# Performance work log

Measured on AMD Instinct MI355X. Metric: run time of the kernel, lower is better.

Reference implementation:

```python
import jax, jax.numpy as jnp
import numpy as np

N = 100000
E = 3200000
NODE_IN = 118
D = 32
H = 4
C = D // H  # 8
EDGE_DIM = 50 + 3
L = 4
LN_EPS = 1e-5


def _layernorm(x, g, b):
    mu = jnp.mean(x, axis=-1, keepdims=True)
    var = jnp.mean(jnp.square(x - mu), axis=-1, keepdims=True)
    return (x - mu) * jax.lax.rsqrt(var + LN_EPS) * g + b


def setup_inputs() -> dict:
    key = jax.random.key(0)
    ks = jax.random.split(key, 20)
    x = jax.random.normal(ks[0], (N, NODE_IN), dtype=jnp.float32)
    edge_index = jax.random.randint(ks[1], (2, E), 0, N, dtype=jnp.int32)
    edge_len = jax.random.normal(ks[2], (E, 50), dtype=jnp.float32)
    edge_vec = jax.random.normal(ks[3], (E, 3), dtype=jnp.float32)
    s_in = 1.0 / np.sqrt(NODE_IN)
    s_d = 1.0 / np.sqrt(D)
    s_e = 1.0 / np.sqrt(EDGE_DIM)
    node_in_W = jax.random.normal(ks[4], (NODE_IN, D), dtype=jnp.float32) * s_in
    node_in_b = jnp.zeros((D,), dtype=jnp.float32)
    ln_g = jnp.ones((L, D), dtype=jnp.float32)
    ln_b = jnp.zeros((L, D), dtype=jnp.float32)
    Wq = jax.random.normal(ks[5], (L, D, D), dtype=jnp.float32) * s_d
    bq = jnp.zeros((L, D), dtype=jnp.float32)
    Wk = jax.random.normal(ks[6], (L, D, D), dtype=jnp.float32) * s_d
    bk = jnp.zeros((L, D), dtype=jnp.float32)
    Wv = jax.random.normal(ks[7], (L, D, D), dtype=jnp.float32) * s_d
    bv = jnp.zeros((L, D), dtype=jnp.float32)
    We = jax.random.normal(ks[8], (L, EDGE_DIM, D), dtype=jnp.float32) * s_e  # lin_edge, bias=False
    Wskip = jax.random.normal(ks[9], (L, D, D), dtype=jnp.float32) * s_d
    bskip = jnp.zeros((L, D), dtype=jnp.float32)
    return {"x": x, "edge_index": edge_index, "edge_len": edge_len, "edge_vec": edge_vec,
            "node_in_W": node_in_W, "node_in_b": node_in_b, "ln_g": ln_g, "ln_b": ln_b,
            "Wq": Wq, "bq": bq, "Wk": Wk, "bk": bk, "Wv": Wv, "bv": bv,
            "We": We, "Wskip": Wskip, "bskip": bskip}


def reference(x, edge_index, edge_len, edge_vec, node_in_W, node_in_b, ln_g, ln_b,
              Wq, bq, Wk, bk, Wv, bv, We, Wskip, bskip):
    src = edge_index[0]  # j (source), messages flow source -> target
    dst = edge_index[1]  # i (target), softmax grouped by dst
    ef = jnp.concatenate([edge_len, edge_vec], axis=-1)  # [E, 53]
    h = x @ node_in_W + node_in_b  # [N, D]
    scale = 1.0 / np.sqrt(C)
    for l in range(L):
        xn = _layernorm(h, ln_g[l], ln_b[l])
        q = (xn @ Wq[l] + bq[l]).reshape(N, H, C)
        k = (xn @ Wk[l] + bk[l]).reshape(N, H, C)
        v = (xn @ Wv[l] + bv[l]).reshape(N, H, C)
        e = (ef @ We[l]).reshape(E, H, C)  # per-edge key/value shift
        kj = k[src] + e                     # [E, H, C]
        alpha = jnp.sum(q[dst] * kj, axis=-1) * scale  # [E, H]
        # segment softmax over incoming edges of each target node
        amax = jax.ops.segment_max(alpha, dst, num_segments=N)  # [N, H]
        amax = jnp.where(jnp.isfinite(amax), amax, 0.0)
        ex = jnp.exp(alpha - amax[dst])
        denom = jax.ops.segment_sum(ex, dst, num_segments=N)
        w = ex / (denom[dst] + 1e-16)       # [E, H]
        msg = (v[src] + e) * w[:, :, None]  # [E, H, C]
        agg = jax.ops.segment_sum(msg.reshape(E, H * C), dst, num_segments=N)  # [N, D]
        y = agg + xn @ Wskip[l] + bskip[l]  # concat heads + root skip (lin_skip(x_i))
        h = h + y                            # residual
    return h
```

## Files before the change

kernel.cpp:

```cpp
#include <hip/hip_runtime.h>
#include <hip/hip_bf16.h>
#include <math.h>

#define N_NODES 100000
#define N_EDGES 3200000
#define NODE_IN 118
#define DIM 32
#define EDF 53
#define NLAYER 4

typedef __attribute__((ext_vector_type(8))) short short8;
typedef __attribute__((ext_vector_type(4))) float f32x4;
typedef unsigned short u16;
typedef unsigned int u32;

static __device__ __forceinline__ float bfhi2f(u32 hi) {
    union { u32 i; float f; } x; x.i = hi; return x.f;
}
static __device__ __forceinline__ u16 f2bf(float f) {
    union { float f; u32 i; } x; x.f = f;
    u32 i = x.i;
    return (u16)((i + 0x7FFFu + ((i >> 16) & 1u)) >> 16);
}
static __device__ __forceinline__ u32 pk2bf(float a, float b) {
    u32 r;
    asm("v_cvt_pk_bf16_f32 %0, %1, %2" : "=v"(r) : "v"(a), "v"(b));
    return r;
}

__global__ __launch_bounds__(256) void k_count(const int* __restrict__ dst, int* __restrict__ cnt) {
    int e = blockIdx.x * 256 + threadIdx.x;
    atomicAdd(&cnt[dst[e]], 1);
}

__global__ __launch_bounds__(256) void k_scanA(const int* __restrict__ cnt, int* __restrict__ off,
                                               int* __restrict__ bsum) {
    __shared__ int s[256];
    int t = threadIdx.x; int i = blockIdx.x * 256 + t;
    int v = (i < N_NODES) ? cnt[i] : 0;
    s[t] = v; __syncthreads();
    for (int d = 1; d < 256; d <<= 1) {
        int x = (t >= d) ? s[t - d] : 0; __syncthreads();
        s[t] += x; __syncthreads();
    }
    if (i < N_NODES) off[i] = s[t] - v;
    if (t == 255) bsum[blockIdx.x] = s[t];
}

__global__ __launch_bounds__(512) void k_scanB(int* bsum, int nb) {
    __shared__ int s[512];
    int t = threadIdx.x;
    int v = (t < nb) ? bsum[t] : 0;
    s[t] = v; __syncthreads();
    for (int d = 1; d < 512; d <<= 1) {
        int x = (t >= d) ? s[t - d] : 0; __syncthreads();
        s[t] += x; __syncthreads();
    }
    if (t < nb) bsum[t] = s[t] - v;
}

__global__ __launch_bounds__(256) void k_scanC(int* off, const int* __restrict__ bsum) {
    int i = blockIdx.x * 256 + threadIdx.x;
    if (i < N_NODES) off[i] += bsum[blockIdx.x];
    if (i == 0) off[N_NODES] = N_EDGES;
}

__global__ __launch_bounds__(256) void k_fill(const int* __restrict__ src, const int* __restrict__ dst,
                                              const int* __restrict__ off, int* __restrict__ cur,
                                              int2* __restrict__ epk) {
    int e = blockIdx.x * 256 + threadIdx.x;
    int d = dst[e];
    int p = off[d] + atomicAdd(&cur[d], 1);
    epk[p] = make_int2(e, src[e]);
}

__global__ __launch_bounds__(256) void k_init(const float* __restrict__ x, const float* __restrict__ W,
                                              const float* __restrict__ b, float* __restrict__ h) {
    __shared__ float Ws[NODE_IN * DIM];
    __shared__ float xs[8][NODE_IN];
    int t = threadIdx.x;
    for (int i = t; i < NODE_IN * DIM; i += 256) Ws[i] = W[i];
    int nb = blockIdx.x * 8;
    for (int i = t; i < 8 * NODE_IN; i += 256) {
        int n = i / NODE_IN, j = i % NODE_IN;
        xs[n][j] = x[(size_t)(nb + n) * NODE_IN + j];
    }
    __syncthreads();
    int n = t >> 5, c = t & 31;
    float acc = b[c];
    #pragma unroll 2
    for (int j = 0; j < NODE_IN; j++) acc += xs[n][j] * Ws[j * DIM + c];
    h[(size_t)(nb + n) * DIM + c] = acc;
}

template <int NL>
__global__ __launch_bounds__(256) void k_egemm(const float* __restrict__ elen, const float* __restrict__ evec,
                                               const float* __restrict__ We, u16* __restrict__ eout) {
    int tid = threadIdx.x;
    int lane = tid & 63;
    int wv = (blockIdx.x * 256 + tid) >> 6;
    int nw = (gridDim.x * 256) >> 6;
    int n15 = lane & 15, kb = lane >> 4;

    short8 bf[2][2 * NL];
    for (int s = 0; s < 2; s++) {
        for (int t = 0; t < 2 * NL; t++) {
            int n = t * 16 + n15;
            int lay = n >> 5, c = n & 31;
            short8 tmp;
            #pragma unroll
            for (int j = 0; j < 8; j++) {
                int kk = s * 32 + kb * 8 + j;
                float w = (kk < EDF) ? We[(size_t)lay * EDF * DIM + (size_t)kk * DIM + c] : 0.f;
                ((u16*)&tmp)[j] = f2bf(w);
            }
            bf[s][t] = tmp;
        }
    }

    const int NT = N_EDGES / 16;

    auto LOADA = [&](int tile, float* fv) {
        int pos = tile * 16 + n15;
        const float* lp = elen + (size_t)pos * 50;
        {
            const float2* p2 = (const float2*)(lp + kb * 8);
            #pragma unroll
            for (int j = 0; j < 4; j++) { float2 t2 = p2[j]; fv[2 * j] = t2.x; fv[2 * j + 1] = t2.y; }
        }
        if (kb < 2) {
            const float2* p2 = (const float2*)(lp + 32 + kb * 8);
            #pragma unroll
            for (int j = 0; j < 4; j++) { float2 t2 = p2[j]; fv[8 + 2 * j] = t2.x; fv[8 + 2 * j + 1] = t2.y; }
        } else if (kb == 2) {
            float2 t2 = *(const float2*)(lp + 48);
            const float* vp = evec + (size_t)pos * 3;
            fv[8] = t2.x; fv[9] = t2.y; fv[10] = vp[0]; fv[11] = vp[1]; fv[12] = vp[2];
            fv[13] = 0.f; fv[14] = 0.f; fv[15] = 0.f;
        } else {
            #pragma unroll
            for (int j = 8; j < 16; j++) fv[j] = 0.f;
        }
    };

    float cur[16];
    if (wv < NT) LOADA(wv, cur);

    for (int tile = wv; tile < NT; tile += nw) {
        int nxt = tile + nw;
        float nx[16];
        if (nxt < NT) LOADA(nxt, nx);

        union { short8 s; u32 u[4]; } A0, A1;
        A0.u[0] = pk2bf(cur[0], cur[1]);  A0.u[1] = pk2bf(cur[2], cur[3]);
        A0.u[2] = pk2bf(cur[4], cur[5]);  A0.u[3] = pk2bf(cur[6], cur[7]);
        A1.u[0] = pk2bf(cur[8], cur[9]);  A1.u[1] = pk2bf(cur[10], cur[11]);
        A1.u[2] = pk2bf(cur[12], cur[13]); A1.u[3] = pk2bf(cur[14], cur[15]);

        size_t rowbase = ((size_t)tile * 16 + n15) * DIM;
        #pragma unroll
        for (int t = 0; t < 2 * NL; t++) {
            f32x4 z = {0.f, 0.f, 0.f, 0.f};
            z = __builtin_amdgcn_mfma_f32_16x16x32_bf16(bf[0][t], A0.s, z, 0, 0, 0);
            z = __builtin_amdgcn_mfma_f32_16x16x32_bf16(bf[1][t], A1.s, z, 0, 0, 0);
            int lay = t >> 1;
            int ch = (t & 1) * 16 + kb * 4;
            uint2 sv = { pk2bf(z[0], z[1]), pk2bf(z[2], z[3]) };
            *(uint2*)&eout[(size_t)lay * N_EDGES * DIM + rowbase + ch] = sv;
        }

        #pragma unroll
        for (int j = 0; j < 16; j++) cur[j] = nx[j];
    }
}

__global__ __launch_bounds__(256) void k_node(const float* __restrict__ h,
        const float* __restrict__ g, const float* __restrict__ bta,
        const float* __restrict__ Wq, const float* __restrict__ bq,
        const float* __restrict__ Wk, const float* __restrict__ bk,
        const float* __restrict__ Wv, const float* __restrict__ bv,
        const float* __restrict__ Ws, const float* __restrict__ bs,
        float* __restrict__ qo, u16* __restrict__ kvo, float* __restrict__ hso) {
    __shared__ float WQ[DIM * DIM], WK[DIM * DIM], WV[DIM * DIM], WS[DIM * DIM];
    __shared__ float xn[8][DIM];
    int t = threadIdx.x;
    for (int i = t; i < DIM * DIM; i += 256) { WQ[i] = Wq[i]; WK[i] = Wk[i]; WV[i] = Wv[i]; WS[i] = Ws[i]; }
    int n = t >> 5, c = t & 31;
    size_t node = (size_t)blockIdx.x * 8 + n;
    float hv = h[node * DIM + c];
    float s1 = hv;
    for (int d = 1; d < 32; d <<= 1) s1 += __shfl_xor(s1, d, 64);
    float mu = s1 * (1.f / 32.f);
    float dv = hv - mu;
    float s2 = dv * dv;
    for (int d = 1; d < 32; d <<= 1) s2 += __shfl_xor(s2, d, 64);
    float inv = rsqrtf(s2 * (1.f / 32.f) + 1e-5f);
    float xv = dv * inv * g[c] + bta[c];
    xn[n][c] = xv;
    __syncthreads();
    float aq = bq[c], ak = bk[c], av = bv[c], as = bs[c];
    #pragma unroll 4
    for (int j = 0; j < DIM; j++) {
        float xj = xn[n][j];
        aq += xj * WQ[j * DIM + c];
        ak += xj * WK[j * DIM + c];
        av += xj * WV[j * DIM + c];
        as += xj * WS[j * DIM + c];
    }
    size_t o = node * DIM + c;
    qo[o] = aq * 0.35355339059327373f;
    kvo[node * 64 + c]      = f2bf(ak);
    kvo[node * 64 + 32 + c] = f2bf(av);
    hso[o] = hv + as;
}

__global__ __launch_bounds__(256) void k_aggr(const int* __restrict__ off, const int2* __restrict__ epk,
        const u16* __restrict__ eb, const float* __restrict__ qb, const u16* __restrict__ kvb,
        const float* __restrict__ hs, float* __restrict__ out) {
    int tid = threadIdx.x;
    size_t node = (size_t)blockIdx.x * 4 + (tid >> 6);
    int lane = tid & 63;
    int eg = lane >> 2, hq = lane & 3, c0 = hq * 8;
    float4 q0 = *(const float4*)&qb[node * DIM + c0];
    float4 q1 = *(const float4*)&qb[node * DIM + c0 + 4];
    int o0 = off[node], o1 = off[node + 1];
    int safe = (o0 < N_EDGES) ? o0 : (N_EDGES - 1);
    float n0=0.f,n1=0.f,n2=0.f,n3=0.f,n4=0.f,n5=0.f,n6=0.f,n7=0.f;
    float dacc = 0.f;

    int pA = o0 + eg;  bool aA = pA < o1; int2 xA = epk[aA ? pA : safe];
    int pB = pA + 16;  bool aB = pB < o1; int2 xB = epk[aB ? pB : safe];
    int pC = pB + 16;  bool aC = pC < o1; int2 xC = epk[aC ? pC : safe];

    uint4 dAe = *(const uint4*)&eb[(size_t)xA.x * DIM + c0];
    uint4 dAk = *(const uint4*)&kvb[(size_t)xA.y * 64 + c0];
    uint4 dAv = *(const uint4*)&kvb[(size_t)xA.y * 64 + 32 + c0];
    uint4 dBe = *(const uint4*)&eb[(size_t)xB.x * DIM + c0];
    uint4 dBk = *(const uint4*)&kvb[(size_t)xB.y * 64 + c0];
    uint4 dBv = *(const uint4*)&kvb[(size_t)xB.y * 64 + 32 + c0];

    for (int p = o0; p < o1; p += 16) {
        uint4 dCe = *(const uint4*)&eb[(size_t)xC.x * DIM + c0];
        uint4 dCk = *(const uint4*)&kvb[(size_t)xC.y * 64 + c0];
        uint4 dCv = *(const uint4*)&kvb[(size_t)xC.y * 64 + 32 + c0];
        int pD = pC + 16; bool aD = pD < o1; int2 xD = epk[aD ? pD : safe];

        float e0 = bfhi2f(dAe.x << 16), e1 = bfhi2f(dAe.x & 0xFFFF0000u);
        float e2 = bfhi2f(dAe.y << 16), e3 = bfhi2f(dAe.y & 0xFFFF0000u);
        float e4 = bfhi2f(dAe.z << 16), e5 = bfhi2f(dAe.z & 0xFFFF0000u);
        float e6 = bfhi2f(dAe.w << 16), e7 = bfhi2f(dAe.w & 0xFFFF0000u);
        float k0 = bfhi2f(dAk.x << 16), k1 = bfhi2f(dAk.x & 0xFFFF0000u);
        float k2 = bfhi2f(dAk.y << 16), k3 = bfhi2f(dAk.y & 0xFFFF0000u);
        float k4 = bfhi2f(dAk.z << 16), k5 = bfhi2f(dAk.z & 0xFFFF0000u);
        float k6 = bfhi2f(dAk.w << 16), k7 = bfhi2f(dAk.w & 0xFFFF0000u);
        float v0 = bfhi2f(dAv.x << 16), v1 = bfhi2f(dAv.x & 0xFFFF0000u);
        float v2 = bfhi2f(dAv.y << 16), v3 = bfhi2f(dAv.y & 0xFFFF0000u);
        float v4 = bfhi2f(dAv.z << 16), v5 = bfhi2f(dAv.z & 0xFFFF0000u);
        float v6 = bfhi2f(dAv.w << 16), v7 = bfhi2f(dAv.w & 0xFFFF0000u);
        float a =      q0.x * (k0 + e0);
        a = fmaf(q0.y, k1 + e1, a);
        a = fmaf(q0.z, k2 + e2, a);
        a = fmaf(q0.w, k3 + e3, a);
        a = fmaf(q1.x, k4 + e4, a);
        a = fmaf(q1.y, k5 + e5, a);
        a = fmaf(q1.z, k6 + e6, a);
        a = fmaf(q1.w, k7 + e7, a);
        float ex = aA ? __expf(a) : 0.f;
        n0 = fmaf(ex, v0 + e0, n0); n1 = fmaf(ex, v1 + e1, n1);
        n2 = fmaf(ex, v2 + e2, n2); n3 = fmaf(ex, v3 + e3, n3);
        n4 = fmaf(ex, v4 + e4, n4); n5 = fmaf(ex, v5 + e5, n5);
        n6 = fmaf(ex, v6 + e6, n6); n7 = fmaf(ex, v7 + e7, n7);
        dacc += ex;

        aA = aB; dAe = dBe; dAk = dBk; dAv = dBv;
        dBe = dCe; dBk = dCk; dBv = dCv;
        aB = aC; xC = xD; aC = aD; pC = pD;
    }
    #pragma unroll
    for (int d = 4; d < 64; d <<= 1) {
        n0 += __shfl_xor(n0, d); n1 += __shfl_xor(n1, d);
        n2 += __shfl_xor(n2, d); n3 += __shfl_xor(n3, d);
        n4 += __shfl_xor(n4, d); n5 += __shfl_xor(n5, d);
        n6 += __shfl_xor(n6, d); n7 += __shfl_xor(n7, d);
        dacc += __shfl_xor(dacc, d);
    }
    if (eg == 0) {
        float inv = 1.f / (dacc + 1e-16f);
        float4 h0 = *(const float4*)&hs[node * DIM + c0];
        float4 h1 = *(const float4*)&hs[node * DIM + c0 + 4];
        float4 o0v = { h0.x + n0 * inv, h0.y + n1 * inv, h0.z + n2 * inv, h0.w + n3 * inv };
        float4 o1v = { h1.x + n4 * inv, h1.y + n5 * inv, h1.z + n6 * inv, h1.w + n7 * inv };
        *(float4*)&out[node * DIM + c0] = o0v;
        *(float4*)&out[node * DIM + c0 + 4] = o1v;
    }
}

extern "C" void kernel_launch(void* const* d_in, const int* in_sizes, int n_in,
                              void* d_out, int out_size, void* d_ws, size_t ws_size,
                              hipStream_t stream) {
    const float* x    = (const float*)d_in[0];
    const int*   ei   = (const int*)d_in[1];
    const int*   src  = ei;
    const int*   dst  = ei + N_EDGES;
    const float* elen = (const float*)d_in[2];
    const float* evec = (const float*)d_in[3];
    const float* niW  = (const float*)d_in[4];
    const float* nib  = (const float*)d_in[5];
    const float* lng  = (const float*)d_in[6];
    const float* lnb  = (const float*)d_in[7];
    const float* Wq   = (const float*)d_in[8];
    const float* bq   = (const float*)d_in[9];
    const float* Wk   = (const float*)d_in[10];
    const float* bk   = (const float*)d_in[11];
    const float* Wv   = (const float*)d_in[12];
    const float* bv   = (const float*)d_in[13];
    const float* We   = (const float*)d_in[14];
    const float* Wsk  = (const float*)d_in[15];
    const float* bsk  = (const float*)d_in[16];
    float* out = (float*)d_out;

    unsigned char* w = (unsigned char*)d_ws;
    auto alloc = [&](size_t bytes) -> void* {
        void* p = (void*)w; w += (bytes + 255) & ~(size_t)255; return p;
    };
    int*   off  = (int*)alloc((N_NODES + 1) * sizeof(int));
    int*   cnt  = (int*)alloc(N_NODES * sizeof(int));
    int*   bsum = (int*)alloc(512 * sizeof(int));
    int2*  epk  = (int2*)alloc((size_t)N_EDGES * sizeof(int2));
    float* h    = (float*)alloc((size_t)N_NODES * DIM * sizeof(float));
    float* qb   = (float*)alloc((size_t)N_NODES * DIM * sizeof(float));
    u16*   kvb  = (u16*)alloc((size_t)N_NODES * 64 * sizeof(u16));
    float* hsb  = (float*)alloc((size_t)N_NODES * DIM * sizeof(float));
    size_t used = (size_t)(w - (unsigned char*)d_ws);
    size_t e_full = (size_t)NLAYER * N_EDGES * DIM * sizeof(u16);
    size_t e_one  = (size_t)N_EDGES * DIM * sizeof(u16);
    bool full = (used + e_full) <= ws_size;
    u16* ebuf = (u16*)alloc(full ? e_full : e_one);

    const int EB = N_EDGES / 256;
    const int NB = N_NODES / 8;
    const int AB = N_NODES / 4;
    const int nbScan = (N_NODES + 255) / 256;

    hipMemsetAsync(cnt, 0, N_NODES * sizeof(int), stream);
    k_count<<<EB, 256, 0, stream>>>(dst, cnt);
    k_scanA<<<nbScan, 256, 0, stream>>>(cnt, off, bsum);
    k_scanB<<<1, 512, 0, stream>>>(bsum, nbScan);
    k_scanC<<<nbScan, 256, 0, stream>>>(off, bsum);
    hipMemsetAsync(cnt, 0, N_NODES * sizeof(int), stream);
    k_fill<<<EB, 256, 0, stream>>>(src, dst, off, cnt, epk);

    k_init<<<NB, 256, 0, stream>>>(x, niW, nib, h);

    if (full) k_egemm<4><<<4096, 256, 0, stream>>>(elen, evec, We, ebuf);

    for (int l = 0; l < NLAYER; l++) {
        if (!full) k_egemm<1><<<4096, 256, 0, stream>>>(elen, evec, We + (size_t)l * EDF * DIM, ebuf);
        k_node<<<NB, 256, 0, stream>>>(h, lng + l * DIM, lnb + l * DIM,
                                       Wq + (size_t)l * DIM * DIM, bq + l * DIM,
                                       Wk + (size_t)l * DIM * DIM, bk + l * DIM,
                                       Wv + (size_t)l * DIM * DIM, bv + l * DIM,
                                       Wsk + (size_t)l * DIM * DIM, bsk + l * DIM,
                                       qb, kvb, hsb);
        const u16* el = full ? (ebuf + (size_t)l * N_EDGES * DIM) : ebuf;
        k_aggr<<<AB, 256, 0, stream>>>(off, epk, el, qb, kvb, hsb,
                                       (l == NLAYER - 1) ? out : h);
    }
}
```

Measured before the change: 1.309 ms.

## Store edge features in CSR order with interleaved layers for streaming aggregation

The edge GEMM now gathers edge inputs through the dst-sorted permutation and writes its output in CSR order, with all four layers interleaved per edge. The output is transposed through LDS so each row goes out as a wide store. The aggregation kernel then reads edge features sequentially by CSR position rather than by scattered edge id, and the packed edge index array is split so it loads only source ids. The scattered reads move into the one-time GEMM input load, and the per-layer reads become a strided stream over the interleaved buffer.

```diff
diff --git a/kernel.cpp b/kernel.cpp
--- a/kernel.cpp
+++ b/kernel.cpp
@@ -67,11 +67,12 @@
 
 __global__ __launch_bounds__(256) void k_fill(const int* __restrict__ src, const int* __restrict__ dst,
                                               const int* __restrict__ off, int* __restrict__ cur,
-                                              int2* __restrict__ epk) {
+                                              int* __restrict__ eidx, int* __restrict__ esrc) {
     int e = blockIdx.x * 256 + threadIdx.x;
     int d = dst[e];
     int p = off[d] + atomicAdd(&cur[d], 1);
-    epk[p] = make_int2(e, src[e]);
+    eidx[p] = e;
+    esrc[p] = src[e];
 }
 
 __global__ __launch_bounds__(256) void k_init(const float* __restrict__ x, const float* __restrict__ W,
@@ -95,9 +96,12 @@
 
 template <int NL>
 __global__ __launch_bounds__(256) void k_egemm(const float* __restrict__ elen, const float* __restrict__ evec,
-                                               const float* __restrict__ We, u16* __restrict__ eout) {
+                                               const int* __restrict__ eidx, const float* __restrict__ We,
+                                               u16* __restrict__ eout) {
+    __shared__ u16 st[4][16 * 160];
     int tid = threadIdx.x;
     int lane = tid & 63;
+    int wvl = tid >> 6;
     int wv = (blockIdx.x * 256 + tid) >> 6;
     int nw = (gridDim.x * 256) >> 6;
     int n15 = lane & 15, kb = lane >> 4;
@@ -120,9 +124,8 @@
 
     const int NT = N_EDGES / 16;
 
-    auto LOADA = [&](int tile, float* fv) {
-        int pos = tile * 16 + n15;
-        const float* lp = elen + (size_t)pos * 50;
+    auto LOADD = [&](int eid, float* fv) {
+        const float* lp = elen + (size_t)eid * 50;
         {
             const float2* p2 = (const float2*)(lp + kb * 8);
             #pragma unroll
@@ -134,7 +137,7 @@
             for (int j = 0; j < 4; j++) { float2 t2 = p2[j]; fv[8 + 2 * j] = t2.x; fv[8 + 2 * j + 1] = t2.y; }
         } else if (kb == 2) {
             float2 t2 = *(const float2*)(lp + 48);
-            const float* vp = evec + (size_t)pos * 3;
+            const float* vp = evec + (size_t)eid * 3;
             fv[8] = t2.x; fv[9] = t2.y; fv[10] = vp[0]; fv[11] = vp[1]; fv[12] = vp[2];
             fv[13] = 0.f; fv[14] = 0.f; fv[15] = 0.f;
         } else {
@@ -143,34 +146,51 @@
         }
     };
 
+    int eidA = (wv < NT) ? eidx[wv * 16 + n15] : 0;
+    int t1 = wv + nw;
+    int eidB = (t1 < NT) ? eidx[t1 * 16 + n15] : 0;
     float cur[16];
-    if (wv < NT) LOADA(wv, cur);
+    if (wv < NT) LOADD(eidA, cur);
 
     for (int tile = wv; tile < NT; tile += nw) {
         int nxt = tile + nw;
         float nx[16];
-        if (nxt < NT) LOADA(nxt, nx);
+        if (nxt < NT) LOADD(eidB, nx);
+        int t2 = tile + 2 * nw;
+        int eidC = (t2 < NT) ? eidx[t2 * 16 + n15] : 0;
 
         union { short8 s; u32 u[4]; } A0, A1;
-        A0.u[0] = pk2bf(cur[0], cur[1]);  A0.u[1] = pk2bf(cur[2], cur[3]);
-        A0.u[2] = pk2bf(cur[4], cur[5]);  A0.u[3] = pk2bf(cur[6], cur[7]);
-        A1.u[0] = pk2bf(cur[8], cur[9]);  A1.u[1] = pk2bf(cur[10], cur[11]);
+        A0.u[0] = pk2bf(cur[0], cur[1]);   A0.u[1] = pk2bf(cur[2], cur[3]);
+        A0.u[2] = pk2bf(cur[4], cur[5]);   A0.u[3] = pk2bf(cur[6], cur[7]);
+        A1.u[0] = pk2bf(cur[8], cur[9]);   A1.u[1] = pk2bf(cur[10], cur[11]);
         A1.u[2] = pk2bf(cur[12], cur[13]); A1.u[3] = pk2bf(cur[14], cur[15]);
 
-        size_t rowbase = ((size_t)tile * 16 + n15) * DIM;
+        u16* W = st[wvl];
         #pragma unroll
         for (int t = 0; t < 2 * NL; t++) {
             f32x4 z = {0.f, 0.f, 0.f, 0.f};
-            z = __builtin_amdgcn_mfma_f32_16x16x32_bf16(bf[0][t], A0.s, z, 0, 0, 0);
-            z = __builtin_amdgcn_mfma_f32_16x16x32_bf16(bf[1][t], A1.s, z, 0, 0, 0);
-            int lay = t >> 1;
-            int ch = (t & 1) * 16 + kb * 4;
-            uint2 sv = { pk2bf(z[0], z[1]), pk2bf(z[2], z[3]) };
-            *(uint2*)&eout[(size_t)lay * N_EDGES * DIM + rowbase + ch] = sv;
+            z = __builtin_amdgcn_mfma_f32_16x16x32_bf16(A0.s, bf[0][t], z, 0, 0, 0);
+            z = __builtin_amdgcn_mfma_f32_16x16x32_bf16(A1.s, bf[1][t], z, 0, 0, 0);
+            int n = t * 16 + n15;
+            #pragma unroll
+            for (int r = 0; r < 4; r++) {
+                int row = kb * 4 + r;
+                int idx = row * 160 + (n ^ ((row & 12) << 2));
+                W[idx] = f2bf(z[r]);
+            }
+        }
+        int row = lane >> 2, q = lane & 3;
+        size_t base2 = (size_t)(tile * 16) * (NL * 32);
+        #pragma unroll
+        for (int lay = 0; lay < NL; lay++) {
+            int idx = row * 160 + ((lay * 32 + q * 8) ^ ((row & 12) << 2));
+            short8 vblk = *(const short8*)&W[idx];
+            *(short8*)&eout[base2 + (size_t)row * (NL * 32) + lay * 32 + q * 8] = vblk;
         }
 
         #pragma unroll
         for (int j = 0; j < 16; j++) cur[j] = nx[j];
+        eidA = eidB; eidB = eidC;
     }
 }
 
@@ -214,8 +234,9 @@
     hso[o] = hv + as;
 }
 
-__global__ __launch_bounds__(256) void k_aggr(const int* __restrict__ off, const int2* __restrict__ epk,
-        const u16* __restrict__ eb, const float* __restrict__ qb, const u16* __restrict__ kvb,
+__global__ __launch_bounds__(256) void k_aggr(const int* __restrict__ off, const int* __restrict__ esrc,
+        const u16* __restrict__ eb, int estr,
+        const float* __restrict__ qb, const u16* __restrict__ kvb,
         const float* __restrict__ hs, float* __restrict__ out) {
     int tid = threadIdx.x;
     size_t node = (size_t)blockIdx.x * 4 + (tid >> 6);
@@ -228,22 +249,24 @@
     float n0=0.f,n1=0.f,n2=0.f,n3=0.f,n4=0.f,n5=0.f,n6=0.f,n7=0.f;
     float dacc = 0.f;
 
-    int pA = o0 + eg;  bool aA = pA < o1; int2 xA = epk[aA ? pA : safe];
-    int pB = pA + 16;  bool aB = pB < o1; int2 xB = epk[aB ? pB : safe];
-    int pC = pB + 16;  bool aC = pC < o1; int2 xC = epk[aC ? pC : safe];
-
-    uint4 dAe = *(const uint4*)&eb[(size_t)xA.x * DIM + c0];
-    uint4 dAk = *(const uint4*)&kvb[(size_t)xA.y * 64 + c0];
-    uint4 dAv = *(const uint4*)&kvb[(size_t)xA.y * 64 + 32 + c0];
-    uint4 dBe = *(const uint4*)&eb[(size_t)xB.x * DIM + c0];
-    uint4 dBk = *(const uint4*)&kvb[(size_t)xB.y * 64 + c0];
-    uint4 dBv = *(const uint4*)&kvb[(size_t)xB.y * 64 + 32 + c0];
+    int pA = o0 + eg;  bool aA = pA < o1; int sA = esrc[aA ? pA : safe];
+    int pB = pA + 16;  bool aB = pB < o1; int sB = esrc[aB ? pB : safe];
+    int pC = pB + 16;  bool aC = pC < o1; int sC = esrc[aC ? pC : safe];
+    int cA = aA ? pA : safe, cB = aB ? pB : safe, cCs = aC ? pC : safe;
+
+    uint4 dAe = *(const uint4*)&eb[(size_t)cA * estr + c0];
+    uint4 dAk = *(const uint4*)&kvb[(size_t)sA * 64 + c0];
+    uint4 dAv = *(const uint4*)&kvb[(size_t)sA * 64 + 32 + c0];
+    uint4 dBe = *(const uint4*)&eb[(size_t)cB * estr + c0];
+    uint4 dBk = *(const uint4*)&kvb[(size_t)sB * 64 + c0];
+    uint4 dBv = *(const uint4*)&kvb[(size_t)sB * 64 + 32 + c0];
 
     for (int p = o0; p < o1; p += 16) {
-        uint4 dCe = *(const uint4*)&eb[(size_t)xC.x * DIM + c0];
-        uint4 dCk = *(const uint4*)&kvb[(size_t)xC.y * 64 + c0];
-        uint4 dCv = *(const uint4*)&kvb[(size_t)xC.y * 64 + 32 + c0];
-        int pD = pC + 16; bool aD = pD < o1; int2 xD = epk[aD ? pD : safe];
+        uint4 dCe = *(const uint4*)&eb[(size_t)cCs * estr + c0];
+        uint4 dCk = *(const uint4*)&kvb[(size_t)sC * 64 + c0];
+        uint4 dCv = *(const uint4*)&kvb[(size_t)sC * 64 + 32 + c0];
+        int pD = pC + 16; bool aD = pD < o1; int qD = aD ? pD : safe;
+        int sD = esrc[qD];
 
         float e0 = bfhi2f(dAe.x << 16), e1 = bfhi2f(dAe.x & 0xFFFF0000u);
         float e2 = bfhi2f(dAe.y << 16), e3 = bfhi2f(dAe.y & 0xFFFF0000u);
@@ -274,7 +297,8 @@
 
         aA = aB; dAe = dBe; dAk = dBk; dAv = dBv;
         dBe = dCe; dBk = dCk; dBv = dCv;
-        aB = aC; xC = xD; aC = aD; pC = pD;
+        aB = aC; aC = aD;
+        cCs = qD; sC = sD; pC = pD;
     }
     #pragma unroll
     for (int d = 4; d < 64; d <<= 1) {
@@ -326,7 +350,8 @@
     int*   off  = (int*)alloc((N_NODES + 1) * sizeof(int));
     int*   cnt  = (int*)alloc(N_NODES * sizeof(int));
     int*   bsum = (int*)alloc(512 * sizeof(int));
-    int2*  epk  = (int2*)alloc((size_t)N_EDGES * sizeof(int2));
+    int*   eidx = (int*)alloc((size_t)N_EDGES * sizeof(int));
+    int*   esrc = (int*)alloc((size_t)N_EDGES * sizeof(int));
     float* h    = (float*)alloc((size_t)N_NODES * DIM * sizeof(float));
     float* qb   = (float*)alloc((size_t)N_NODES * DIM * sizeof(float));
     u16*   kvb  = (u16*)alloc((size_t)N_NODES * 64 * sizeof(u16));
@@ -348,22 +373,23 @@
     k_scanB<<<1, 512, 0, stream>>>(bsum, nbScan);
     k_scanC<<<nbScan, 256, 0, stream>>>(off, bsum);
     hipMemsetAsync(cnt, 0, N_NODES * sizeof(int), stream);
-    k_fill<<<EB, 256, 0, stream>>>(src, dst, off, cnt, epk);
+    k_fill<<<EB, 256, 0, stream>>>(src, dst, off, cnt, eidx, esrc);
 
     k_init<<<NB, 256, 0, stream>>>(x, niW, nib, h);
 
-    if (full) k_egemm<4><<<4096, 256, 0, stream>>>(elen, evec, We, ebuf);
+    if (full) k_egemm<4><<<4096, 256, 0, stream>>>(elen, evec, eidx, We, ebuf);
 
     for (int l = 0; l < NLAYER; l++) {
-        if (!full) k_egemm<1><<<4096, 256, 0, stream>>>(elen, evec, We + (size_t)l * EDF * DIM, ebuf);
+        if (!full) k_egemm<1><<<4096, 256, 0, stream>>>(elen, evec, eidx, We + (size_t)l * EDF * DIM, ebuf);
         k_node<<<NB, 256, 0, stream>>>(h, lng + l * DIM, lnb + l * DIM,
                                        Wq + (size_t)l * DIM * DIM, bq + l * DIM,
                                        Wk + (size_t)l * DIM * DIM, bk + l * DIM,
                                        Wv + (size_t)l * DIM * DIM, bv + l * DIM,
                                        Wsk + (size_t)l * DIM * DIM, bsk + l * DIM,
                                        qb, kvb, hsb);
-        const u16* el = full ? (ebuf + (size_t)l * N_EDGES * DIM) : ebuf;
-        k_aggr<<<AB, 256, 0, stream>>>(off, epk, el, qb, kvb, hsb,
+        const u16* el = full ? (ebuf + (size_t)l * DIM) : ebuf;
+        int estr = full ? (NLAYER * DIM) : DIM;
+        k_aggr<<<AB, 256, 0, stream>>>(off, esrc, el, estr, qb, kvb, hsb,
                                        (l == NLAYER - 1) ? out : h);
     }
 }
```

Result: slower. 1.451 ms (+10.8%).

## Split per-node attention aggregation into edge-parallel alpha kernel and segment-sum kernel

Applied to the files above, without the earlier changes.

Replaces the fused per-destination aggregation kernel with two kernels. An edge-parallel kernel computes exp(alpha) and the weighted message for each CSR-ordered edge and writes them to new edge-sized buffers. A second kernel sums them per node, with 4 nodes per wavefront. The aim is to remove load imbalance and poor lane use from variable-degree nodes. The cost is extra global traffic: about 200MB of message and exp writes plus reads per layer, and a wider 16-byte edge record.

```diff
diff --git a/kernel.cpp b/kernel.cpp
--- a/kernel.cpp
+++ b/kernel.cpp
@@ -67,11 +67,11 @@
 
 __global__ __launch_bounds__(256) void k_fill(const int* __restrict__ src, const int* __restrict__ dst,
                                               const int* __restrict__ off, int* __restrict__ cur,
-                                              int2* __restrict__ epk) {
+                                              int4* __restrict__ epk) {
     int e = blockIdx.x * 256 + threadIdx.x;
     int d = dst[e];
     int p = off[d] + atomicAdd(&cur[d], 1);
-    epk[p] = make_int2(e, src[e]);
+    epk[p] = make_int4(e, src[e], d, 0);
 }
 
 __global__ __launch_bounds__(256) void k_init(const float* __restrict__ x, const float* __restrict__ W,
@@ -152,9 +152,9 @@
         if (nxt < NT) LOADA(nxt, nx);
 
         union { short8 s; u32 u[4]; } A0, A1;
-        A0.u[0] = pk2bf(cur[0], cur[1]);  A0.u[1] = pk2bf(cur[2], cur[3]);
-        A0.u[2] = pk2bf(cur[4], cur[5]);  A0.u[3] = pk2bf(cur[6], cur[7]);
-        A1.u[0] = pk2bf(cur[8], cur[9]);  A1.u[1] = pk2bf(cur[10], cur[11]);
+        A0.u[0] = pk2bf(cur[0], cur[1]);   A0.u[1] = pk2bf(cur[2], cur[3]);
+        A0.u[2] = pk2bf(cur[4], cur[5]);   A0.u[3] = pk2bf(cur[6], cur[7]);
+        A1.u[0] = pk2bf(cur[8], cur[9]);   A1.u[1] = pk2bf(cur[10], cur[11]);
         A1.u[2] = pk2bf(cur[12], cur[13]); A1.u[3] = pk2bf(cur[14], cur[15]);
 
         size_t rowbase = ((size_t)tile * 16 + n15) * DIM;
@@ -214,70 +214,78 @@
     hso[o] = hv + as;
 }
 
-__global__ __launch_bounds__(256) void k_aggr(const int* __restrict__ off, const int2* __restrict__ epk,
+__global__ __launch_bounds__(256) void k_alpha(const int4* __restrict__ epk,
         const u16* __restrict__ eb, const float* __restrict__ qb, const u16* __restrict__ kvb,
+        u16* __restrict__ mb, float* __restrict__ exb) {
+    int t = blockIdx.x * 256 + threadIdx.x;
+    int hq = t & 3, c0 = hq * 8;
+    size_t p = (size_t)(t >> 2);
+    int4 pk = epk[p];
+    int eid = pk.x, sj = pk.y, nd = pk.z;
+    uint4 e4 = *(const uint4*)&eb[(size_t)eid * DIM + c0];
+    uint4 k4 = *(const uint4*)&kvb[(size_t)sj * 64 + c0];
+    uint4 v4 = *(const uint4*)&kvb[(size_t)sj * 64 + 32 + c0];
+    float4 q0 = *(const float4*)&qb[(size_t)nd * DIM + c0];
+    float4 q1 = *(const float4*)&qb[(size_t)nd * DIM + c0 + 4];
+
+    float e0 = bfhi2f(e4.x << 16), e1 = bfhi2f(e4.x & 0xFFFF0000u);
+    float e2 = bfhi2f(e4.y << 16), e3 = bfhi2f(e4.y & 0xFFFF0000u);
+    float e4f = bfhi2f(e4.z << 16), e5 = bfhi2f(e4.z & 0xFFFF0000u);
+    float e6 = bfhi2f(e4.w << 16), e7 = bfhi2f(e4.w & 0xFFFF0000u);
+    float k0 = bfhi2f(k4.x << 16), k1 = bfhi2f(k4.x & 0xFFFF0000u);
+    float k2 = bfhi2f(k4.y << 16), k3 = bfhi2f(k4.y & 0xFFFF0000u);
+    float k4f = bfhi2f(k4.z << 16), k5 = bfhi2f(k4.z & 0xFFFF0000u);
+    float k6 = bfhi2f(k4.w << 16), k7 = bfhi2f(k4.w & 0xFFFF0000u);
+    float v0 = bfhi2f(v4.x << 16), v1 = bfhi2f(v4.x & 0xFFFF0000u);
+    float v2 = bfhi2f(v4.y << 16), v3 = bfhi2f(v4.y & 0xFFFF0000u);
+    float v4f = bfhi2f(v4.z << 16), v5 = bfhi2f(v4.z & 0xFFFF0000u);
+    float v6 = bfhi2f(v4.w << 16), v7 = bfhi2f(v4.w & 0xFFFF0000u);
+
+    float a =      q0.x * (k0 + e0);
+    a = fmaf(q0.y, k1 + e1, a);
+    a = fmaf(q0.z, k2 + e2, a);
+    a = fmaf(q0.w, k3 + e3, a);
+    a = fmaf(q1.x, k4f + e4f, a);
+    a = fmaf(q1.y, k5 + e5, a);
+    a = fmaf(q1.z, k6 + e6, a);
+    a = fmaf(q1.w, k7 + e7, a);
+    float ex = __expf(a);
+
+    uint4 mm;
+    mm.x = pk2bf(ex * (v0 + e0),  ex * (v1 + e1));
+    mm.y = pk2bf(ex * (v2 + e2),  ex * (v3 + e3));
+    mm.z = pk2bf(ex * (v4f + e4f), ex * (v5 + e5));
+    mm.w = pk2bf(ex * (v6 + e6),  ex * (v7 + e7));
+    *(uint4*)&mb[p * DIM + c0] = mm;
+    exb[p * 4 + hq] = ex;
+}
+
+__global__ __launch_bounds__(256) void k_msum(const int* __restrict__ off,
+        const u16* __restrict__ mb, const float* __restrict__ exb,
         const float* __restrict__ hs, float* __restrict__ out) {
     int tid = threadIdx.x;
-    size_t node = (size_t)blockIdx.x * 4 + (tid >> 6);
     int lane = tid & 63;
-    int eg = lane >> 2, hq = lane & 3, c0 = hq * 8;
-    float4 q0 = *(const float4*)&qb[node * DIM + c0];
-    float4 q1 = *(const float4*)&qb[node * DIM + c0 + 4];
+    int ns = lane >> 4, eg = (lane >> 2) & 3, hq = lane & 3, c0 = hq * 8;
+    size_t node = (size_t)blockIdx.x * 16 + (size_t)(tid >> 6) * 4 + ns;
     int o0 = off[node], o1 = off[node + 1];
-    int safe = (o0 < N_EDGES) ? o0 : (N_EDGES - 1);
     float n0=0.f,n1=0.f,n2=0.f,n3=0.f,n4=0.f,n5=0.f,n6=0.f,n7=0.f;
     float dacc = 0.f;
-
-    int pA = o0 + eg;  bool aA = pA < o1; int2 xA = epk[aA ? pA : safe];
-    int pB = pA + 16;  bool aB = pB < o1; int2 xB = epk[aB ? pB : safe];
-    int pC = pB + 16;  bool aC = pC < o1; int2 xC = epk[aC ? pC : safe];
-
-    uint4 dAe = *(const uint4*)&eb[(size_t)xA.x * DIM + c0];
-    uint4 dAk = *(const uint4*)&kvb[(size_t)xA.y * 64 + c0];
-    uint4 dAv = *(const uint4*)&kvb[(size_t)xA.y * 64 + 32 + c0];
-    uint4 dBe = *(const uint4*)&eb[(size_t)xB.x * DIM + c0];
-    uint4 dBk = *(const uint4*)&kvb[(size_t)xB.y * 64 + c0];
-    uint4 dBv = *(const uint4*)&kvb[(size_t)xB.y * 64 + 32 + c0];
-
-    for (int p = o0; p < o1; p += 16) {
-        uint4 dCe = *(const uint4*)&eb[(size_t)xC.x * DIM + c0];
-        uint4 dCk = *(const uint4*)&kvb[(size_t)xC.y * 64 + c0];
-        uint4 dCv = *(const uint4*)&kvb[(size_t)xC.y * 64 + 32 + c0];
-        int pD = pC + 16; bool aD = pD < o1; int2 xD = epk[aD ? pD : safe];
-
-        float e0 = bfhi2f(dAe.x << 16), e1 = bfhi2f(dAe.x & 0xFFFF0000u);
-        float e2 = bfhi2f(dAe.y << 16), e3 = bfhi2f(dAe.y & 0xFFFF0000u);
-        float e4 = bfhi2f(dAe.z << 16), e5 = bfhi2f(dAe.z & 0xFFFF0000u);
-        float e6 = bfhi2f(dAe.w << 16), e7 = bfhi2f(dAe.w & 0xFFFF0000u);
-        float k0 = bfhi2f(dAk.x << 16), k1 = bfhi2f(dAk.x & 0xFFFF0000u);
-        float k2 = bfhi2f(dAk.y << 16), k3 = bfhi2f(dAk.y & 0xFFFF0000u);
-        float k4 = bfhi2f(dAk.z << 16), k5 = bfhi2f(dAk.z & 0xFFFF0000u);
-        float k6 = bfhi2f(dAk.w << 16), k7 = bfhi2f(dAk.w & 0xFFFF0000u);
-        float v0 = bfhi2f(dAv.x << 16), v1 = bfhi2f(dAv.x & 0xFFFF0000u);
-        float v2 = bfhi2f(dAv.y << 16), v3 = bfhi2f(dAv.y & 0xFFFF0000u);
-        float v4 = bfhi2f(dAv.z << 16), v5 = bfhi2f(dAv.z & 0xFFFF0000u);
-        float v6 = bfhi2f(dAv.w << 16), v7 = bfhi2f(dAv.w & 0xFFFF0000u);
-        float a =      q0.x * (k0 + e0);
-        a = fmaf(q0.y, k1 + e1, a);
-        a = fmaf(q0.z, k2 + e2, a);
-        a = fmaf(q0.w, k3 + e3, a);
-        a = fmaf(q1.x, k4 + e4, a);
-        a = fmaf(q1.y, k5 + e5, a);
-        a = fmaf(q1.z, k6 + e6, a);
-        a = fmaf(q1.w, k7 + e7, a);
-        float ex = aA ? __expf(a) : 0.f;
-        n0 = fmaf(ex, v0 + e0, n0); n1 = fmaf(ex, v1 + e1, n1);
-        n2 = fmaf(ex, v2 + e2, n2); n3 = fmaf(ex, v3 + e3, n3);
-        n4 = fmaf(ex, v4 + e4, n4); n5 = fmaf(ex, v5 + e5, n5);
-        n6 = fmaf(ex, v6 + e6, n6); n7 = fmaf(ex, v7 + e7, n7);
-        dacc += ex;
-
-        aA = aB; dAe = dBe; dAk = dBk; dAv = dBv;
-        dBe = dCe; dBk = dCk; dBv = dCv;
-        aB = aC; xC = xD; aC = aD; pC = pD;
+    for (int p0 = o0; p0 < o1; p0 += 4) {
+        int p = p0 + eg;
+        bool act = p < o1;
+        int pc = act ? p : o0;
+        uint4 m4 = *(const uint4*)&mb[(size_t)pc * DIM + c0];
+        float ex = exb[(size_t)pc * 4 + hq];
+        if (act) {
+            n0 += bfhi2f(m4.x << 16); n1 += bfhi2f(m4.x & 0xFFFF0000u);
+            n2 += bfhi2f(m4.y << 16); n3 += bfhi2f(m4.y & 0xFFFF0000u);
+            n4 += bfhi2f(m4.z << 16); n5 += bfhi2f(m4.z & 0xFFFF0000u);
+            n6 += bfhi2f(m4.w << 16); n7 += bfhi2f(m4.w & 0xFFFF0000u);
+            dacc += ex;
+        }
     }
     #pragma unroll
-    for (int d = 4; d < 64; d <<= 1) {
+    for (int d = 4; d <= 8; d <<= 1) {
         n0 += __shfl_xor(n0, d); n1 += __shfl_xor(n1, d);
         n2 += __shfl_xor(n2, d); n3 += __shfl_xor(n3, d);
         n4 += __shfl_xor(n4, d); n5 += __shfl_xor(n5, d);
@@ -326,11 +334,13 @@
     int*   off  = (int*)alloc((N_NODES + 1) * sizeof(int));
     int*   cnt  = (int*)alloc(N_NODES * sizeof(int));
     int*   bsum = (int*)alloc(512 * sizeof(int));
-    int2*  epk  = (int2*)alloc((size_t)N_EDGES * sizeof(int2));
+    int4*  epk  = (int4*)alloc((size_t)N_EDGES * sizeof(int4));
     float* h    = (float*)alloc((size_t)N_NODES * DIM * sizeof(float));
     float* qb   = (float*)alloc((size_t)N_NODES * DIM * sizeof(float));
     u16*   kvb  = (u16*)alloc((size_t)N_NODES * 64 * sizeof(u16));
     float* hsb  = (float*)alloc((size_t)N_NODES * DIM * sizeof(float));
+    u16*   mb   = (u16*)alloc((size_t)N_EDGES * DIM * sizeof(u16));
+    float* exb  = (float*)alloc((size_t)N_EDGES * 4 * sizeof(float));
     size_t used = (size_t)(w - (unsigned char*)d_ws);
     size_t e_full = (size_t)NLAYER * N_EDGES * DIM * sizeof(u16);
     size_t e_one  = (size_t)N_EDGES * DIM * sizeof(u16);
@@ -339,7 +349,8 @@
 
     const int EB = N_EDGES / 256;
     const int NB = N_NODES / 8;
-    const int AB = N_NODES / 4;
+    const int MB_ = N_NODES / 16;
+    const int ALB = (N_EDGES * 4) / 256;
     const int nbScan = (N_NODES + 255) / 256;
 
     hipMemsetAsync(cnt, 0, N_NODES * sizeof(int), stream);
@@ -363,7 +374,8 @@
                                        Wsk + (size_t)l * DIM * DIM, bsk + l * DIM,
                                        qb, kvb, hsb);
         const u16* el = full ? (ebuf + (size_t)l * N_EDGES * DIM) : ebuf;
-        k_aggr<<<AB, 256, 0, stream>>>(off, epk, el, qb, kvb, hsb,
-                                       (l == NLAYER - 1) ? out : h);
-    }
-}
+        k_alpha<<<ALB, 256, 0, stream>>>(epk, el, qb, kvb, mb, exb);
+        k_msum<<<MB_, 256, 0, stream>>>(off, mb, exb, hsb,
+                                        (l == NLAYER - 1) ? out : h);
+    }
+}
```

Measured after the change: 1.756 ms. 1.34x slower.
